# Kernel tuning notes

Measured on AMD Instinct MI355X. Metric: run time of the kernel, lower is better.

The kernel has to match this reference:

```python
import jax, jax.numpy as jnp
import numpy as np

EMBED = 1024
HEADS = 16
HEAD_DIM = EMBED // HEADS


def setup_inputs() -> dict:
    key = jax.random.key(0)
    ks = jax.random.split(key, 12)
    B, S, D = 4, 2048, EMBED
    scale = 1.0 / np.sqrt(D)
    inp = {
        "query": jax.random.normal(ks[0], (B, S, D), dtype=jnp.float32),
        "key": jax.random.normal(ks[1], (B, S, D), dtype=jnp.float32),
        "value": jax.random.normal(ks[2], (B, S, D), dtype=jnp.float32),
        "Wq": jax.random.normal(ks[3], (D, D), dtype=jnp.float32) * scale,
        "bq": jnp.zeros((D,), dtype=jnp.float32),
        "Wk": jax.random.normal(ks[4], (D, D), dtype=jnp.float32) * scale,
        "bk": jnp.zeros((D,), dtype=jnp.float32),
        "Wv": jax.random.normal(ks[5], (D, D), dtype=jnp.float32) * scale,
        "bv": jnp.zeros((D,), dtype=jnp.float32),
        "Wo": jax.random.normal(ks[6], (D, D), dtype=jnp.float32) * scale,
        "bo": jnp.zeros((D,), dtype=jnp.float32),
    }
    return inp


def reference(query, key, value, Wq, bq, Wk, bk, Wv, bv, Wo, bo):
    B, S, D = query.shape
    H, Dh = HEADS, HEAD_DIM

    def proj(x, W, b):
        # nn.Linear: x @ W.T + b, then split heads -> [B, H, S, Dh]
        y = jnp.einsum('bsd,ed->bse', x, W) + b
        return y.reshape(B, -1, H, Dh).transpose(0, 2, 1, 3)

    q = proj(query, Wq, bq)
    k = proj(key, Wk, bk)
    v = proj(value, Wv, bv)

    attn = jnp.einsum('bhqd,bhkd->bhqk', q, k) / jnp.sqrt(jnp.float32(Dh))
    attn = jax.nn.softmax(attn, axis=-1)
    # dropout: eval mode -> identity
    out = jnp.einsum('bhqk,bhkd->bhqd', attn, v)
    out = out.transpose(0, 2, 1, 3).reshape(B, -1, D)
    out = jnp.einsum('bsd,ed->bse', out, Wo) + bo
    return out
```

## Files before the change

### kernel.cpp

```cpp
#include <hip/hip_runtime.h>
#include <hip/hip_bf16.h>

typedef unsigned short u16;
typedef unsigned int u32;
typedef float f32x4 __attribute__((ext_vector_type(4)));
typedef float f32x16 __attribute__((ext_vector_type(16)));
typedef __bf16 bf16x8 __attribute__((ext_vector_type(8)));
typedef u32 u32x2 __attribute__((ext_vector_type(2)));

#define DEV static __device__ __forceinline__

DEV u16 f2b(float f) { __bf16 h = (__bf16)f; u16 r; __builtin_memcpy(&r, &h, 2); return r; }
DEV u32 pk2(float a, float b) { return (u32)f2b(a) | ((u32)f2b(b) << 16); }
DEV bf16x8 as_bf(uint4 v) { bf16x8 r; __builtin_memcpy(&r, &v, 16); return r; }

#define GLDS(g, l) __builtin_amdgcn_global_load_lds( \
    (__attribute__((address_space(1))) void*)(g),     \
    (__attribute__((address_space(3))) void*)(l), 16, 0, 0)

DEV void wb2()  { asm volatile("s_waitcnt vmcnt(2)\n\ts_barrier" ::: "memory"); }
DEV void wb4()  { asm volatile("s_waitcnt vmcnt(4)\n\ts_barrier" ::: "memory"); }
DEV void wb0()  { asm volatile("s_waitcnt vmcnt(0)\n\ts_barrier" ::: "memory"); }
DEV void wb0l() { asm volatile("s_waitcnt vmcnt(0) lgkmcnt(0)\n\ts_barrier" ::: "memory"); }

__global__ __launch_bounds__(256) void convw_k(const float* __restrict__ w0,
                                               const float* __restrict__ w1,
                                               const float* __restrict__ w2,
                                               const float* __restrict__ w3,
                                               u16* __restrict__ dst)
{
  const int seg = blockIdx.x >> 9, sb = blockIdx.x & 511;
  const float* s = seg == 0 ? w0 : seg == 1 ? w1 : seg == 2 ? w2 : w3;
  const int i = sb * 256 + threadIdx.x;
  const float4* p = (const float4*)(s + (size_t)i * 8);
  const float4 a = p[0], b = p[1];
  *(uint4*)(dst + (size_t)seg * 1048576 + (size_t)i * 8) =
      make_uint4(pk2(a.x, a.y), pk2(a.z, a.w), pk2(b.x, b.y), pk2(b.z, b.w));
}

__global__ __launch_bounds__(256) void gemm_qkv(const float* __restrict__ Aq,
                                                const float* __restrict__ Ak,
                                                const float* __restrict__ Av,
                                                const u16* __restrict__ Wc,
                                                const float* __restrict__ bq,
                                                const float* __restrict__ bk,
                                                const float* __restrict__ bv,
                                                u16* __restrict__ Qw,
                                                u16* __restrict__ Kw,
                                                u16* __restrict__ Vw,
                                                float qscale)
{
  __shared__ u16 lds[3][8192];
  const int tid = threadIdx.x;
  const int lane = tid & 63, w = tid >> 6;
  const int z = blockIdx.z;
  const int m0 = blockIdx.x * 128, e0 = blockIdx.y * 128;
  const int wrb = (w >> 1) * 4, wcb = (w & 1) * 4;

  const float* Af = z == 0 ? Aq : (z == 1 ? Ak : Av);
  const u16* Wp = Wc + (size_t)z * 1048576;
  const float* bias = z == 0 ? bq : (z == 1 ? bk : bv);
  u16* Cp = z == 0 ? Qw : (z == 1 ? Kw : Vw);
  const float scale = z == 0 ? qscale : 1.0f;
  const int cmode = (z == 2) ? 3 : 2;

  f32x4 acc[4][4];
#pragma unroll
  for (int i = 0; i < 4; i++)
#pragma unroll
    for (int j = 0; j < 4; j++)
#pragma unroll
      for (int r = 0; r < 4; r++) acc[i][j][r] = 0.f;

  const float* gAf = Af + (size_t)(m0 + w * 32 + (lane & 15)) * 1024 + (lane >> 4) * 8;
  const u16*   gB  = Wp + (size_t)(e0 + w * 32 + (lane & 15)) * 1024 + (lane >> 4) * 8;
  const int aoff = w * 1024 + (lane >> 4) * 128 + (lane & 15) * 8;

  float4 fA0, fA1, fA2, fA3;

#define GSB(K0, BUF)                                           \
  GLDS(gB + (K0),         &lds[BUF][4096 + w * 1024]);         \
  GLDS(gB + (K0) + 16384, &lds[BUF][4096 + w * 1024 + 512]);

#define LOAD_A(K0)                                             \
  { const float* s0 = gAf + (K0); const float* s1 = s0 + 16384; \
    fA0 = ((const float4*)s0)[0]; fA1 = ((const float4*)s0)[1]; \
    fA2 = ((const float4*)s1)[0]; fA3 = ((const float4*)s1)[1]; }

#define WRITE_A(BUF)                                                          \
  { *(uint4*)&lds[BUF][aoff] = make_uint4(pk2(fA0.x, fA0.y), pk2(fA0.z, fA0.w), \
                                          pk2(fA1.x, fA1.y), pk2(fA1.z, fA1.w)); \
    *(uint4*)&lds[BUF][aoff + 512] = make_uint4(pk2(fA2.x, fA2.y), pk2(fA2.z, fA2.w), \
                                                pk2(fA3.x, fA3.y), pk2(fA3.z, fA3.w)); }

  const int fo = (lane >> 4) * 128 + (lane & 15) * 8;

#define GEMM_STEP(BUF)                                                         \
  {                                                                            \
    const u16* la = &lds[BUF][0];                                              \
    const u16* lb = &lds[BUF][4096];                                           \
    bf16x8 af[4], bfr[4];                                                      \
    _Pragma("unroll")                                                          \
    for (int i = 0; i < 4; i++) {                                              \
      af[i]  = as_bf(*(const uint4*)(la + (wrb + i) * 512 + fo));              \
      bfr[i] = as_bf(*(const uint4*)(lb + (wcb + i) * 512 + fo));              \
    }                                                                          \
    _Pragma("unroll")                                                          \
    for (int i = 0; i < 4; i++)                                                \
      _Pragma("unroll")                                                        \
      for (int j = 0; j < 4; j++)                                              \
        acc[i][j] = __builtin_amdgcn_mfma_f32_16x16x32_bf16(af[i], bfr[j],     \
                                                            acc[i][j], 0, 0, 0); \
  }

  GSB(0, 0)
  LOAD_A(0)
  WRITE_A(0)
  GSB(32, 1)
  LOAD_A(32)

  for (int t = 0; t < 30; t += 3) {
    wb0l(); GSB((t + 2) * 32, 2) WRITE_A(1) LOAD_A((t + 2) * 32) GEMM_STEP(0)
    wb0l(); GSB((t + 3) * 32, 0) WRITE_A(2) LOAD_A((t + 3) * 32) GEMM_STEP(1)
    wb0l(); GSB((t + 4) * 32, 1) WRITE_A(0) LOAD_A((t + 4) * 32) GEMM_STEP(2)
  }
  wb0l(); WRITE_A(1) GEMM_STEP(0)
  wb0l(); GEMM_STEP(1)
#undef GEMM_STEP
#undef WRITE_A
#undef LOAD_A
#undef GSB

  const int col = lane & 15, rb4 = (lane >> 4) * 4;
  const int wr = wrb * 16, wc = wcb * 16;
#pragma unroll
  for (int j = 0; j < 4; j++) {
    const int e = e0 + wc + j * 16 + col;
    const float bv2 = bias[e];
#pragma unroll
    for (int i = 0; i < 4; i++) {
#pragma unroll
      for (int r = 0; r < 4; r++) {
        const int m = m0 + wr + i * 16 + rb4 + r;
        const float v = (acc[i][j][r] + bv2) * scale;
        const int b = m >> 11, s = m & 2047, h = e >> 6, dh = e & 63;
        const size_t bh = (size_t)(b * 16 + h);
        if (cmode == 2) {
          const size_t idx = (((bh * 64 + (s >> 5)) * 4 + (dh >> 4)) * 64
                              + ((dh >> 3) & 1) * 32 + (s & 31)) * 8 + (dh & 7);
          Cp[idx] = f2b(v);
        } else {
          const size_t idx = ((bh * 64 + (s >> 5)) * 8 + ((s >> 4) & 1) * 4
                              + (dh >> 5) * 2 + ((s >> 3) & 1)) * 256
                             + (size_t)(dh & 31) * 8 + (s & 7);
          Cp[idx] = f2b(v);
        }
      }
    }
  }
}

__global__ __launch_bounds__(256) void gemm_o(const u16* __restrict__ A,
                                              const u16* __restrict__ W,
                                              const float* __restrict__ bias,
                                              float* __restrict__ Cp)
{
  __shared__ u16 lds[3][8192];
  const int tid = threadIdx.x;
  const int lane = tid & 63, w = tid >> 6;
  const int m0 = blockIdx.x * 128, e0 = blockIdx.y * 128;
  const int wrb = (w >> 1) * 4, wcb = (w & 1) * 4;

  f32x4 acc[4][4];
#pragma unroll
  for (int i = 0; i < 4; i++)
#pragma unroll
    for (int j = 0; j < 4; j++)
#pragma unroll
      for (int r = 0; r < 4; r++) acc[i][j][r] = 0.f;

  const u16* gA = A + (size_t)(m0 + w * 32 + (lane & 15)) * 1024 + (lane >> 4) * 8;
  const u16* gB = W + (size_t)(e0 + w * 32 + (lane & 15)) * 1024 + (lane >> 4) * 8;

#define GSTAGE(K0, BUF)                                        \
  GLDS(gA + (K0),         &lds[BUF][w * 1024]);                \
  GLDS(gA + (K0) + 16384, &lds[BUF][w * 1024 + 512]);          \
  GLDS(gB + (K0),         &lds[BUF][4096 + w * 1024]);         \
  GLDS(gB + (K0) + 16384, &lds[BUF][4096 + w * 1024 + 512]);

  GSTAGE(0, 0)
  GSTAGE(32, 1)

  const int fo = (lane >> 4) * 128 + (lane & 15) * 8;

#define GEMM_STEP(BUF)                                                         \
  {                                                                            \
    const u16* la = &lds[BUF][0];                                              \
    const u16* lb = &lds[BUF][4096];                                           \
    bf16x8 af[4], bfr[4];                                                      \
    _Pragma("unroll")                                                          \
    for (int i = 0; i < 4; i++) {                                              \
      af[i]  = as_bf(*(const uint4*)(la + (wrb + i) * 512 + fo));              \
      bfr[i] = as_bf(*(const uint4*)(lb + (wcb + i) * 512 + fo));              \
    }                                                                          \
    _Pragma("unroll")                                                          \
    for (int i = 0; i < 4; i++)                                                \
      _Pragma("unroll")                                                        \
      for (int j = 0; j < 4; j++)                                              \
        acc[i][j] = __builtin_amdgcn_mfma_f32_16x16x32_bf16(af[i], bfr[j],     \
                                                            acc[i][j], 0, 0, 0); \
  }

  for (int t = 0; t < 30; t += 3) {
    wb4(); GSTAGE((t + 2) * 32, 2) GEMM_STEP(0)
    wb4(); GSTAGE((t + 3) * 32, 0) GEMM_STEP(1)
    wb4(); GSTAGE((t + 4) * 32, 1) GEMM_STEP(2)
  }
  wb4(); GEMM_STEP(0)
  wb0(); GEMM_STEP(1)
#undef GEMM_STEP
#undef GSTAGE

  const int col = lane & 15, rb4 = (lane >> 4) * 4;
  const int wr = wrb * 16, wc = wcb * 16;
#pragma unroll
  for (int j = 0; j < 4; j++) {
    const int e = e0 + wc + j * 16 + col;
    const float bv = bias[e];
#pragma unroll
    for (int i = 0; i < 4; i++) {
#pragma unroll
      for (int r = 0; r < 4; r++) {
        const int m = m0 + wr + i * 16 + rb4 + r;
        Cp[(size_t)m * 1024 + e] = acc[i][j][r] + bv;
      }
    }
  }
}

__global__ __launch_bounds__(256, 4) void attn_k(const u16* __restrict__ Qb,
                                                 const u16* __restrict__ Kb,
                                                 const u16* __restrict__ Vb,
                                                 u16* __restrict__ O)
{
  __shared__ u16 pool[12288];
  const int tid = threadIdx.x, wv = tid >> 6, lane = tid & 63;
  const int lo = lane & 31, hi = lane >> 5;
  const int bid = blockIdx.x;
  const int xcd = bid & 7, ix = bid >> 3;
  const int bh = xcd * 8 + (ix & 7);
  const int qb = (ix >> 3) * 4 + wv;
  const int b = bh >> 4, h = bh & 15, q0 = qb * 32;

  const u16* qp = Qb + ((size_t)(bh * 64 + qb) * 4) * 512 + (size_t)lane * 8;
  bf16x8 qf[4];
#pragma unroll
  for (int c = 0; c < 4; c++) qf[c] = as_bf(*(const uint4*)(qp + c * 512));

  f32x16 a0, a1, zv;
#pragma unroll
  for (int r = 0; r < 16; r++) { a0[r] = 0.f; a1[r] = 0.f; zv[r] = 0.f; }
  float ls0 = 0.f, ls1 = 0.f;

  const u16* sgK = Kb + (size_t)bh * 131072 + wv * 512 + (size_t)lane * 8;
  const u16* sgV = Vb + (size_t)bh * 131072 + wv * 512 + (size_t)lane * 8;

#define ASTAGE(T, BUF)                                                  \
  GLDS(sgK + (size_t)(T) * 2048, pool + (BUF) * 4096 + wv * 512);       \
  GLDS(sgV + (size_t)(T) * 2048, pool + (BUF) * 4096 + 2048 + wv * 512);

  ASTAGE(0, 0)
  ASTAGE(1, 1)

#define ATTN_STEP(BUF)                                                        \
  {                                                                           \
    const u16* kl = pool + (BUF) * 4096;                                      \
    const u16* vl = kl + 2048;                                                \
    __builtin_amdgcn_s_setprio(1);                                            \
    f32x16 s = __builtin_amdgcn_mfma_f32_32x32x16_bf16(                       \
                 as_bf(*(const uint4*)(kl + lane * 8)), qf[0], zv, 0, 0, 0);  \
    _Pragma("unroll")                                                         \
    for (int c = 1; c < 4; c++)                                               \
      s = __builtin_amdgcn_mfma_f32_32x32x16_bf16(                            \
            as_bf(*(const uint4*)(kl + c * 512 + lane * 8)), qf[c], s, 0, 0, 0); \
    __builtin_amdgcn_s_setprio(0);                                            \
    _Pragma("unroll")                                                         \
    for (int r = 0; r < 16; r++) s[r] = __builtin_amdgcn_exp2f(s[r]);         \
    _Pragma("unroll")                                                         \
    for (int r = 0; r < 16; r += 2) { ls0 += s[r]; ls1 += s[r + 1]; }         \
    bf16x8 pf[2];                                                             \
    _Pragma("unroll")                                                         \
    for (int kc = 0; kc < 2; kc++) {                                          \
      const u32 A0 = pk2(s[8 * kc + 0], s[8 * kc + 1]);                       \
      const u32 A1 = pk2(s[8 * kc + 2], s[8 * kc + 3]);                       \
      const u32 B0 = pk2(s[8 * kc + 4], s[8 * kc + 5]);                       \
      const u32 B1 = pk2(s[8 * kc + 6], s[8 * kc + 7]);                       \
      u32x2 w02 = __builtin_amdgcn_permlane32_swap(A0, B0, false, false);     \
      u32x2 w13 = __builtin_amdgcn_permlane32_swap(A1, B1, false, false);     \
      pf[kc] = as_bf(make_uint4(w02[0], w13[0], w02[1], w13[1]));             \
    }                                                                         \
    __builtin_amdgcn_s_setprio(1);                                            \
    a0 = __builtin_amdgcn_mfma_f32_32x32x16_bf16(                             \
           as_bf(*(const uint4*)(vl + 0    + lane * 8)), pf[0], a0, 0, 0, 0); \
    a1 = __builtin_amdgcn_mfma_f32_32x32x16_bf16(                             \
           as_bf(*(const uint4*)(vl + 512  + lane * 8)), pf[0], a1, 0, 0, 0); \
    a0 = __builtin_amdgcn_mfma_f32_32x32x16_bf16(                             \
           as_bf(*(const uint4*)(vl + 1024 + lane * 8)), pf[1], a0, 0, 0, 0); \
    a1 = __builtin_amdgcn_mfma_f32_32x32x16_bf16(                             \
           as_bf(*(const uint4*)(vl + 1536 + lane * 8)), pf[1], a1, 0, 0, 0); \
    __builtin_amdgcn_s_setprio(0);                                            \
  }

  for (int t = 0; t < 60; t += 3) {
    wb2(); ASTAGE(t + 2, 2) ATTN_STEP(0)
    wb2(); ASTAGE(t + 3, 0) ATTN_STEP(1)
    wb2(); ASTAGE(t + 4, 1) ATTN_STEP(2)
  }
  wb2(); ASTAGE(62, 2) ATTN_STEP(0)
  wb2(); ASTAGE(63, 0) ATTN_STEP(1)
  wb2(); ATTN_STEP(2)
  wb0(); ATTN_STEP(0)
#undef ATTN_STEP
#undef ASTAGE

  __syncthreads();

  float l = ls0 + ls1;
  l += __shfl_xor(l, 32);
  const float inv = 1.f / l;
  u16* ob = pool + (wv * 32) * 72;

#pragma unroll
  for (int r = 0; r < 16; r++) {
    const int dh = (r & 3) + 8 * (r >> 2) + 4 * hi;
    ob[lo * 72 + dh]      = f2b(a0[r] * inv);
    ob[lo * 72 + dh + 32] = f2b(a1[r] * inv);
  }
  __builtin_amdgcn_s_barrier();
  const int qr = lane >> 1, hf = lane & 1;
  const u16* src = ob + qr * 72 + hf * 32;
  const uint4 r0 = *(const uint4*)(src + 0);
  const uint4 r1 = *(const uint4*)(src + 8);
  const uint4 r2 = *(const uint4*)(src + 16);
  const uint4 r3 = *(const uint4*)(src + 24);
  const size_t m = (size_t)b * 2048 + q0 + qr;
  uint4* dst = (uint4*)(O + m * 1024 + (size_t)h * 64 + hf * 32);
  dst[0] = r0; dst[1] = r1; dst[2] = r2; dst[3] = r3;
}

extern "C" void kernel_launch(void* const* d_in, const int* in_sizes, int n_in,
                              void* d_out, int out_size, void* d_ws, size_t ws_size,
                              hipStream_t stream)
{
  const float* query = (const float*)d_in[0];
  const float* key   = (const float*)d_in[1];
  const float* value = (const float*)d_in[2];
  const float* Wq = (const float*)d_in[3];
  const float* bq = (const float*)d_in[4];
  const float* Wk = (const float*)d_in[5];
  const float* bk = (const float*)d_in[6];
  const float* Wv = (const float*)d_in[7];
  const float* bv = (const float*)d_in[8];
  const float* Wo = (const float*)d_in[9];
  const float* bo = (const float*)d_in[10];

  const size_t MAT = (size_t)8192 * 1024;
  const size_t WMAT = (size_t)1024 * 1024;
  if (ws_size < (4 * MAT + 4 * WMAT) * sizeof(u16)) return;
  u16* Wc = (u16*)d_ws;
  u16* Qw = Wc + 4 * WMAT;
  u16* Kw = Qw + MAT;
  u16* Vw = Kw + MAT;
  u16* Ow = Vw + MAT;

  const float qscale = 0.125f * 1.4426950408889634f;

  dim3 bl(256, 1, 1);
  hipLaunchKernelGGL(convw_k, dim3(2048), bl, 0, stream, Wq, Wk, Wv, Wo, Wc);

  hipLaunchKernelGGL(gemm_qkv, dim3(64, 8, 3), bl, 0, stream,
                     query, key, value, Wc, bq, bk, bv, Qw, Kw, Vw, qscale);

  hipLaunchKernelGGL(attn_k, dim3(1024), bl, 0, stream, Qw, Kw, Vw, Ow);

  hipLaunchKernelGGL(gemm_o, dim3(64, 8), bl, 0, stream,
                     Ow, Wc + 3 * WMAT, bo, (float*)d_out);
}
```

Before: 295.1 us.

## Pre-convert QKV activations to bf16 and load A via direct-to-LDS async copies

Adds a separate kernel that converts query/key/value from fp32 to bf16 in workspace. The QKV GEMM then streams both A and B tiles with global_load_lds, which removes the register-staged fp32 load, convert and LDS-write path. The barrier waits only on older loads (vmcnt(4)), so copies overlap compute more fully. The cost is an extra pass over the activations (fp32 read plus bf16 write and reread) and more workspace, with a sequential per-projection fallback when workspace is small.

Result: faster. 257.7 us (-12.7%).

```diff
diff --git a/kernel.cpp b/kernel.cpp
--- a/kernel.cpp
+++ b/kernel.cpp
@@ -18,10 +18,26 @@
     (__attribute__((address_space(1))) void*)(g),     \
     (__attribute__((address_space(3))) void*)(l), 16, 0, 0)
 
-DEV void wb2()  { asm volatile("s_waitcnt vmcnt(2)\n\ts_barrier" ::: "memory"); }
-DEV void wb4()  { asm volatile("s_waitcnt vmcnt(4)\n\ts_barrier" ::: "memory"); }
-DEV void wb0()  { asm volatile("s_waitcnt vmcnt(0)\n\ts_barrier" ::: "memory"); }
-DEV void wb0l() { asm volatile("s_waitcnt vmcnt(0) lgkmcnt(0)\n\ts_barrier" ::: "memory"); }
+DEV void wb2() { asm volatile("s_waitcnt vmcnt(2)\n\ts_barrier" ::: "memory"); }
+DEV void wb4() { asm volatile("s_waitcnt vmcnt(4)\n\ts_barrier" ::: "memory"); }
+DEV void wb0() { asm volatile("s_waitcnt vmcnt(0)\n\ts_barrier" ::: "memory"); }
+
+__global__ __launch_bounds__(256) void conva3_k(const float* __restrict__ s0,
+                                                const float* __restrict__ s1,
+                                                const float* __restrict__ s2,
+                                                u16* __restrict__ dst, int n8)
+{
+  const int seg = blockIdx.y;
+  const float* s = seg == 0 ? s0 : (seg == 1 ? s1 : s2);
+  u16* d = dst + (size_t)seg * 8388608;
+  const int stride = gridDim.x * 256;
+  for (int i = blockIdx.x * 256 + threadIdx.x; i < n8; i += stride) {
+    const float4* p = (const float4*)(s + (size_t)i * 8);
+    const float4 a = p[0], b = p[1];
+    *(uint4*)(d + (size_t)i * 8) =
+        make_uint4(pk2(a.x, a.y), pk2(a.z, a.w), pk2(b.x, b.y), pk2(b.z, b.w));
+  }
+}
 
 __global__ __launch_bounds__(256) void convw_k(const float* __restrict__ w0,
                                                const float* __restrict__ w1,
@@ -38,17 +54,15 @@
       make_uint4(pk2(a.x, a.y), pk2(a.z, a.w), pk2(b.x, b.y), pk2(b.z, b.w));
 }
 
-__global__ __launch_bounds__(256) void gemm_qkv(const float* __restrict__ Aq,
-                                                const float* __restrict__ Ak,
-                                                const float* __restrict__ Av,
+__global__ __launch_bounds__(256) void gemm_qkv(const u16* __restrict__ Ac,
                                                 const u16* __restrict__ Wc,
-                                                const float* __restrict__ bq,
-                                                const float* __restrict__ bk,
-                                                const float* __restrict__ bv,
-                                                u16* __restrict__ Qw,
-                                                u16* __restrict__ Kw,
-                                                u16* __restrict__ Vw,
-                                                float qscale)
+                                                const float* __restrict__ b0,
+                                                const float* __restrict__ b1,
+                                                const float* __restrict__ b2,
+                                                u16* __restrict__ C0,
+                                                u16* __restrict__ C1,
+                                                u16* __restrict__ C2,
+                                                float qscale, int zq, int zv)
 {
   __shared__ u16 lds[3][8192];
   const int tid = threadIdx.x;
@@ -57,12 +71,12 @@
   const int m0 = blockIdx.x * 128, e0 = blockIdx.y * 128;
   const int wrb = (w >> 1) * 4, wcb = (w & 1) * 4;
 
-  const float* Af = z == 0 ? Aq : (z == 1 ? Ak : Av);
+  const u16* A = Ac + (size_t)z * 8388608;
   const u16* Wp = Wc + (size_t)z * 1048576;
-  const float* bias = z == 0 ? bq : (z == 1 ? bk : bv);
-  u16* Cp = z == 0 ? Qw : (z == 1 ? Kw : Vw);
-  const float scale = z == 0 ? qscale : 1.0f;
-  const int cmode = (z == 2) ? 3 : 2;
+  const float* bias = z == 0 ? b0 : (z == 1 ? b1 : b2);
+  u16* Cp = z == 0 ? C0 : (z == 1 ? C1 : C2);
+  const float scale = (z == zq) ? qscale : 1.0f;
+  const int cmode = (z == zv) ? 3 : 2;
 
   f32x4 acc[4][4];
 #pragma unroll
@@ -72,26 +86,17 @@
 #pragma unroll
       for (int r = 0; r < 4; r++) acc[i][j][r] = 0.f;
 
-  const float* gAf = Af + (size_t)(m0 + w * 32 + (lane & 15)) * 1024 + (lane >> 4) * 8;
-  const u16*   gB  = Wp + (size_t)(e0 + w * 32 + (lane & 15)) * 1024 + (lane >> 4) * 8;
-  const int aoff = w * 1024 + (lane >> 4) * 128 + (lane & 15) * 8;
-
-  float4 fA0, fA1, fA2, fA3;
-
-#define GSB(K0, BUF)                                           \
+  const u16* gA = A  + (size_t)(m0 + w * 32 + (lane & 15)) * 1024 + (lane >> 4) * 8;
+  const u16* gB = Wp + (size_t)(e0 + w * 32 + (lane & 15)) * 1024 + (lane >> 4) * 8;
+
+#define GSTAGE(K0, BUF)                                        \
+  GLDS(gA + (K0),         &lds[BUF][w * 1024]);                \
+  GLDS(gA + (K0) + 16384, &lds[BUF][w * 1024 + 512]);          \
   GLDS(gB + (K0),         &lds[BUF][4096 + w * 1024]);         \
   GLDS(gB + (K0) + 16384, &lds[BUF][4096 + w * 1024 + 512]);
 
-#define LOAD_A(K0)                                             \
-  { const float* s0 = gAf + (K0); const float* s1 = s0 + 16384; \
-    fA0 = ((const float4*)s0)[0]; fA1 = ((const float4*)s0)[1]; \
-    fA2 = ((const float4*)s1)[0]; fA3 = ((const float4*)s1)[1]; }
-
-#define WRITE_A(BUF)                                                          \
-  { *(uint4*)&lds[BUF][aoff] = make_uint4(pk2(fA0.x, fA0.y), pk2(fA0.z, fA0.w), \
-                                          pk2(fA1.x, fA1.y), pk2(fA1.z, fA1.w)); \
-    *(uint4*)&lds[BUF][aoff + 512] = make_uint4(pk2(fA2.x, fA2.y), pk2(fA2.z, fA2.w), \
-                                                pk2(fA3.x, fA3.y), pk2(fA3.z, fA3.w)); }
+  GSTAGE(0, 0)
+  GSTAGE(32, 1)
 
   const int fo = (lane >> 4) * 128 + (lane & 15) * 8;
 
@@ -113,23 +118,15 @@
                                                             acc[i][j], 0, 0, 0); \
   }
 
-  GSB(0, 0)
-  LOAD_A(0)
-  WRITE_A(0)
-  GSB(32, 1)
-  LOAD_A(32)
-
   for (int t = 0; t < 30; t += 3) {
-    wb0l(); GSB((t + 2) * 32, 2) WRITE_A(1) LOAD_A((t + 2) * 32) GEMM_STEP(0)
-    wb0l(); GSB((t + 3) * 32, 0) WRITE_A(2) LOAD_A((t + 3) * 32) GEMM_STEP(1)
-    wb0l(); GSB((t + 4) * 32, 1) WRITE_A(0) LOAD_A((t + 4) * 32) GEMM_STEP(2)
-  }
-  wb0l(); WRITE_A(1) GEMM_STEP(0)
-  wb0l(); GEMM_STEP(1)
+    wb4(); GSTAGE((t + 2) * 32, 2) GEMM_STEP(0)
+    wb4(); GSTAGE((t + 3) * 32, 0) GEMM_STEP(1)
+    wb4(); GSTAGE((t + 4) * 32, 1) GEMM_STEP(2)
+  }
+  wb4(); GEMM_STEP(0)
+  wb0(); GEMM_STEP(1)
 #undef GEMM_STEP
-#undef WRITE_A
-#undef LOAD_A
-#undef GSB
+#undef GSTAGE
 
   const int col = lane & 15, rb4 = (lane >> 4) * 4;
   const int wr = wrb * 16, wc = wcb * 16;
@@ -366,23 +363,53 @@
 
   const size_t MAT = (size_t)8192 * 1024;
   const size_t WMAT = (size_t)1024 * 1024;
-  if (ws_size < (4 * MAT + 4 * WMAT) * sizeof(u16)) return;
-  u16* Wc = (u16*)d_ws;
-  u16* Qw = Wc + 4 * WMAT;
-  u16* Kw = Qw + MAT;
-  u16* Vw = Kw + MAT;
-  u16* Ow = Vw + MAT;
-
   const float qscale = 0.125f * 1.4426950408889634f;
-
   dim3 bl(256, 1, 1);
-  hipLaunchKernelGGL(convw_k, dim3(2048), bl, 0, stream, Wq, Wk, Wv, Wo, Wc);
-
-  hipLaunchKernelGGL(gemm_qkv, dim3(64, 8, 3), bl, 0, stream,
-                     query, key, value, Wc, bq, bk, bv, Qw, Kw, Vw, qscale);
-
-  hipLaunchKernelGGL(attn_k, dim3(1024), bl, 0, stream, Qw, Kw, Vw, Ow);
-
-  hipLaunchKernelGGL(gemm_o, dim3(64, 8), bl, 0, stream,
-                     Ow, Wc + 3 * WMAT, bo, (float*)d_out);
-}
+
+  if (ws_size >= (6 * MAT + 4 * WMAT) * sizeof(u16)) {
+    u16* Ac3 = (u16*)d_ws;
+    u16* Wc  = Ac3 + 3 * MAT;
+    u16* Qw  = Wc + 4 * WMAT;
+    u16* Kw  = Qw + MAT;
+    u16* Vw  = Kw + MAT;
+    u16* Ow  = Ac3;
+
+    hipLaunchKernelGGL(convw_k, dim3(2048), bl, 0, stream, Wq, Wk, Wv, Wo, Wc);
+    hipLaunchKernelGGL(conva3_k, dim3(2048, 3), bl, 0, stream,
+                       query, key, value, Ac3, (int)(MAT / 8));
+    hipLaunchKernelGGL(gemm_qkv, dim3(64, 8, 3), bl, 0, stream,
+                       Ac3, Wc, bq, bk, bv, Qw, Kw, Vw, qscale, 0, 2);
+    hipLaunchKernelGGL(attn_k, dim3(1024), bl, 0, stream, Qw, Kw, Vw, Ow);
+    hipLaunchKernelGGL(gemm_o, dim3(64, 8), bl, 0, stream,
+                       Ow, Wc + 3 * WMAT, bo, (float*)d_out);
+  } else {
+    u16* Ac = (u16*)d_ws;
+    u16* Wc = Ac + MAT;
+    u16* Qw = Wc + 4 * WMAT;
+    u16* Kw = Qw + MAT;
+    u16* Vw = Kw + MAT;
+    u16* Ow = Ac;
+    if (ws_size < (4 * MAT + 4 * WMAT) * sizeof(u16)) return;
+
+    hipLaunchKernelGGL(convw_k, dim3(2048), bl, 0, stream, Wq, Wk, Wv, Wo, Wc);
+
+    hipLaunchKernelGGL(conva3_k, dim3(2048, 1), bl, 0, stream,
+                       query, query, query, Ac, (int)(MAT / 8));
+    hipLaunchKernelGGL(gemm_qkv, dim3(64, 8, 1), bl, 0, stream,
+                       Ac, Wc + 0 * WMAT, bq, bq, bq, Qw, Qw, Qw, qscale, 0, -1);
+
+    hipLaunchKernelGGL(conva3_k, dim3(2048, 1), bl, 0, stream,
+                       key, key, key, Ac, (int)(MAT / 8));
+    hipLaunchKernelGGL(gemm_qkv, dim3(64, 8, 1), bl, 0, stream,
+                       Ac, Wc + 1 * WMAT, bk, bk, bk, Kw, Kw, Kw, qscale, -1, -1);
+
+    hipLaunchKernelGGL(conva3_k, dim3(2048, 1), bl, 0, stream,
+                       value, value, value, Ac, (int)(MAT / 8));
+    hipLaunchKernelGGL(gemm_qkv, dim3(64, 8, 1), bl, 0, stream,
+                       Ac, Wc + 2 * WMAT, bv, bv, bv, Vw, Vw, Vw, qscale, -1, 0);
+
+    hipLaunchKernelGGL(attn_k, dim3(1024), bl, 0, stream, Qw, Kw, Vw, Ow);
+    hipLaunchKernelGGL(gemm_o, dim3(64, 8), bl, 0, stream,
+                       Ow, Wc + 3 * WMAT, bo, (float*)d_out);
+  }
+}
```
